# Kernel tuning notes

Measured on AMD Instinct MI355X. Metric: run time of the kernel, lower is better.

## Reference

```python
import jax, jax.numpy as jnp
import numpy as np

EPS = 1e-5

def _conv(x, w, b=None):
    # NCHW conv, stride 1, padding 1 (SAME for 3x3)
    y = jax.lax.conv_general_dilated(x, w, window_strides=(1, 1),
                                     padding=((1, 1), (1, 1)),
                                     dimension_numbers=('NCHW', 'OIHW', 'NCHW'))
    if b is not None:
        y = y + b[None, :, None, None]
    return y


def setup_inputs() -> dict:
    key = jax.random.key(0)
    ks = jax.random.split(key, 8)
    B, H, W = 4, 512, 640
    depth = jax.random.uniform(ks[0], (B, 1, H, W), dtype=jnp.float32) * 100.0
    img_feature = jax.random.normal(ks[1], (B, 16, H, W), dtype=jnp.float32)
    w1 = jax.random.normal(ks[2], (32, 16, 3, 3), dtype=jnp.float32) * 0.05
    b1 = jax.random.normal(ks[3], (32,), dtype=jnp.float32) * 0.05
    gamma = jnp.ones((32,), dtype=jnp.float32)
    beta = jnp.zeros((32,), dtype=jnp.float32)
    rmean = jax.random.normal(ks[4], (32,), dtype=jnp.float32) * 0.05
    rvar = jax.random.uniform(ks[5], (32,), dtype=jnp.float32) + 0.5
    w2 = jax.random.normal(ks[6], (9, 32, 3, 3), dtype=jnp.float32) * 0.05
    return {"depth": depth, "img_feature": img_feature, "w1": w1, "b1": b1,
            "gamma": gamma, "beta": beta, "rmean": rmean, "rvar": rvar, "w2": w2}


def reference(depth, img_feature, w1, b1, gamma, beta, rmean, rvar, w2):
    B, _, H, W = depth.shape
    # depth_propagation_layer: conv -> BN (eval, running stats) -> relu -> conv
    h1 = _conv(img_feature, w1, b1)
    h1 = (h1 - rmean[None, :, None, None]) * (gamma[None, :, None, None]
          * jax.lax.rsqrt(rvar + EPS)[None, :, None, None]) + beta[None, :, None, None]
    h1 = jax.nn.relu(h1)
    logits = _conv(h1, w2)                    # [B, 9, H, W]
    prob = jax.nn.softmax(logits, axis=1)     # per-pixel 3x3 filter weights
    dp = jnp.pad(depth, ((0, 0), (0, 0), (1, 1), (1, 1)), mode='edge')  # [B,1,H+2,W+2]
    patches = jnp.concatenate([dp[:, :, i:i + H, j:j + W]
                               for i in range(3) for j in range(3)], axis=1)  # [B,9,H,W]
    result_depth = jnp.sum(patches * prob, axis=1)  # [B, H, W]
    return result_depth
```

## Files before the change

kernel.cpp:

```cpp
#include <hip/hip_runtime.h>
#include <hip/hip_bf16.h>

#define HH 512
#define WW 640
#define HW (HH*WW)
#define NT 256
#define IMPLANEP (468*8 + 8)
#define H1PLANEP (360*8 + 8)

typedef short short8  __attribute__((ext_vector_type(8)));
typedef short short4v __attribute__((ext_vector_type(4)));
typedef float f32x16  __attribute__((ext_vector_type(16)));
typedef float f32x4   __attribute__((ext_vector_type(4)));

__device__ inline short f2bf(float f) {
    __hip_bfloat16 h = __float2bfloat16(f);
    short s; __builtin_memcpy(&s, &h, 2);
    return s;
}

__global__ void prep_weights(const float* __restrict__ w1, const float* __restrict__ b1,
                             const float* __restrict__ gamma, const float* __restrict__ beta,
                             const float* __restrict__ rmean, const float* __restrict__ rvar,
                             const float* __restrict__ w2,
                             short* __restrict__ ws_w1, short* __restrict__ ws_w2)
{
    int tid = blockIdx.x*blockDim.x + threadIdx.x;
    int stride = gridDim.x*blockDim.x;
    for (int i = tid; i < 4608; i += stride) {
        int oc = i / 144, rem = i - oc*144, c = rem / 9, t = rem - c*9;
        float a = gamma[oc] * rsqrtf(rvar[oc] + 1e-5f);
        ws_w1[t*512 + oc*16 + c] = f2bf(w1[i] * a);
    }
    for (int i = tid; i < 512; i += stride) {
        int oc = i >> 4, c = i & 15;
        float a = gamma[oc] * rsqrtf(rvar[oc] + 1e-5f);
        float bias = beta[oc] + (b1[oc] - rmean[oc]) * a;
        ws_w1[9*512 + i] = (c == 0) ? f2bf(bias) : (short)0;
    }
    for (int i = tid; i < 4608; i += stride) {
        int t = i >> 9, f = (i >> 5) & 15, c = i & 31;
        float val = (f < 9) ? w2[(f*32 + c)*9 + t] : 0.f;
        ws_w2[i] = f2bf(val);
    }
}

__launch_bounds__(NT, 4)
__global__ void fastprop_main(const float* __restrict__ depth,
                              const float* __restrict__ img,
                              const short* __restrict__ ws_w1,
                              const short* __restrict__ ws_w2,
                              float* __restrict__ out)
{
    __shared__ short s_img[2*IMPLANEP];
    __shared__ short s_h1 [4*H1PLANEP];
    __shared__ float s_depth[340];

    const int tid = threadIdx.x;

    int nid = blockIdx.x;
    int oid = (nid & 7)*640 + (nid >> 3);
    int bz = oid / 1280; int rem = oid - bz*1280;
    int by = rem / 20;   int bx = rem - by*20;
    const int gy0 = by*8, gx0 = bx*32;

    const float* imgb = img   + (size_t)bz*16*HW;
    const float* dpb  = depth + (size_t)bz*HW;

    const int lane = tid & 63;
    const int wid  = tid >> 6;

    const int oc = lane & 31, cg = lane >> 5;
    short8 a1[10];
    #pragma unroll
    for (int t = 0; t < 10; ++t)
        a1[t] = *(const short8*)&ws_w1[t*512 + oc*16 + cg*8];
    short8 bb = (short8)0;
    bb[0] = (cg == 0) ? (short)0x3F80 : (short)0;

    for (int g = tid; g < 936; g += NT) {
        int pixel = g >> 1, half = g & 1;
        int iy = pixel / 36, ix = pixel - iy*36;
        int gy = gy0 + iy - 2, gx = gx0 + ix - 2;
        bool v = ((unsigned)gy < HH) && ((unsigned)gx < WW);
        int cy = min(max(gy, 0), HH-1), cx = min(max(gx, 0), WW-1);
        const float* p = imgb + (size_t)(half*8)*HW + cy*WW + cx;
        float m = v ? 1.f : 0.f;
        short8 vv;
        #pragma unroll
        for (int c = 0; c < 8; ++c) vv[c] = f2bf(m * p[c*HW]);
        *(short8*)&s_img[half*IMPLANEP + pixel*8] = vv;
    }
    #pragma unroll
    for (int it = 0; it < 2; ++it) {
        int idx = tid + it*NT;
        if (idx < 340) {
            int ty = idx / 34, tx = idx - ty*34;
            int gy = min(max(gy0 + ty - 1, 0), HH-1);
            int gx = min(max(gx0 + tx - 1, 0), WW-1);
            s_depth[idx] = dpb[gy*WW + gx];
        }
    }
    __syncthreads();

    {
        const int OFS1[9] = {0, 8, 16, 288, 296, 304, 576, 584, 592};
        const int px = lane & 31;

        #pragma unroll
        for (int gi = 0; gi < 3; ++gi) {
            int g    = wid + gi*4;
            int hp   = g*32 + px;
            int base = cg*IMPLANEP + hp*8;
            f32x16 acc;
            #pragma unroll
            for (int i = 0; i < 16; ++i) acc[i] = 0.f;
            acc = __builtin_amdgcn_mfma_f32_32x32x16_bf16(a1[9], bb, acc, 0, 0, 0);
            #pragma unroll
            for (int t = 0; t < 9; ++t)
                acc = __builtin_amdgcn_mfma_f32_32x32x16_bf16(
                         a1[t], *(const short8*)&s_img[base + OFS1[t]], acc, 0, 0, 0);

            if (hp < 360) {
                unsigned hy = (unsigned)hp / 36u;
                int hx = hp - (int)hy*36;
                int gy = gy0 + (int)hy - 1, gx = gx0 + hx - 1;
                bool inb = ((unsigned)gy < HH) && ((unsigned)gx < WW);
                #pragma unroll
                for (int q = 0; q < 4; ++q) {
                    short4v h;
                    #pragma unroll
                    for (int j = 0; j < 4; ++j) {
                        float hv = fmaxf(acc[q*4 + j], 0.f);
                        h[j] = inb ? f2bf(hv) : (short)0;
                    }
                    *(short4v*)&s_h1[q*H1PLANEP + hp*8 + 4*cg] = h;
                }
            }
        }
    }
    __syncthreads();

    {
        const int fl = lane & 15, cg2 = lane >> 4;
        short8 a2[9];
        #pragma unroll
        for (int t = 0; t < 9; ++t)
            a2[t] = *(const short8*)&ws_w2[t*512 + fl*32 + cg2*8];

        const int r0 = 2*wid;

        #pragma unroll
        for (int chh = 0; chh < 2; ++chh) {
            const int ox0 = chh*16;
            const int colbase = cg2*H1PLANEP + (ox0 + fl)*8;

            short8 F[4][3];
            #pragma unroll
            for (int i = 0; i < 3; ++i)
                #pragma unroll
                for (int dx = 0; dx < 3; ++dx)
                    F[i][dx] = *(const short8*)&s_h1[colbase + ((r0 + i)*36 + dx)*8];
            #pragma unroll
            for (int dx = 0; dx < 3; ++dx)
                F[3][dx] = *(const short8*)&s_h1[colbase + ((r0 + 3)*36 + dx)*8];

            f32x4 acc0, acc1;
            #pragma unroll
            for (int i = 0; i < 4; ++i) { acc0[i] = 0.f; acc1[i] = 0.f; }
            #pragma unroll
            for (int ty = 0; ty < 3; ++ty)
                #pragma unroll
                for (int tx = 0; tx < 3; ++tx)
                    acc0 = __builtin_amdgcn_mfma_f32_16x16x32_bf16(
                             a2[ty*3 + tx], F[ty][tx], acc0, 0, 0, 0);
            #pragma unroll
            for (int ty = 0; ty < 3; ++ty)
                #pragma unroll
                for (int tx = 0; tx < 3; ++tx)
                    acc1 = __builtin_amdgcn_mfma_f32_16x16x32_bf16(
                             a2[ty*3 + tx], F[ty + 1][tx], acc1, 0, 0, 0);

            #pragma unroll
            for (int rr = 0; rr < 2; ++rr) {
                f32x4 lg = rr ? acc1 : acc0;
                int oy = r0 + rr, ox = ox0 + fl;
                float num = 0.f, den = 0.f;
                #pragma unroll
                for (int r = 0; r < 4; ++r) {
                    int f = cg2*4 + r;
                    if (f < 9) {
                        float e = __expf(lg[r]);
                        int fy = f/3, fx = f - fy*3;
                        float d = s_depth[(oy + fy)*34 + (ox + fx)];
                        den += e; num += e * d;
                    }
                }
                num += __shfl_xor(num, 16); den += __shfl_xor(den, 16);
                num += __shfl_xor(num, 32); den += __shfl_xor(den, 32);
                if (cg2 == 0)
                    out[(size_t)bz*HW + (size_t)(gy0 + oy)*WW + (gx0 + ox)] = num / den;
            }
        }
    }
}

extern "C" void kernel_launch(void* const* d_in, const int* in_sizes, int n_in,
                              void* d_out, int out_size, void* d_ws, size_t ws_size,
                              hipStream_t stream) {
    const float* depth = (const float*)d_in[0];
    const float* img   = (const float*)d_in[1];
    const float* w1    = (const float*)d_in[2];
    const float* b1    = (const float*)d_in[3];
    const float* gamma = (const float*)d_in[4];
    const float* beta  = (const float*)d_in[5];
    const float* rmean = (const float*)d_in[6];
    const float* rvar  = (const float*)d_in[7];
    const float* w2    = (const float*)d_in[8];
    float* out = (float*)d_out;

    short* ws_w1 = (short*)d_ws;
    short* ws_w2 = ws_w1 + 5120;

    prep_weights<<<16, NT, 0, stream>>>(w1, b1, gamma, beta, rmean, rvar, w2,
                                        ws_w1, ws_w2);
    fastprop_main<<<5120, NT, 0, stream>>>(depth, img, ws_w1, ws_w2, out);
}
```

Measured before the change: 63.41 us.

## Make blocks persistent over five tiles with register prefetch of next tile

The grid shrinks from 5120 to 1024 blocks, and each block loops over five consecutive tiles. While the current tile's MFMA convolutions and softmax run, the next tile's image and depth values are loaded from global memory into registers. The staged image halo drops from 13 rows to the 12 actually needed, which cuts global loads. This targets global-load latency exposed between the load and compute phases. The cost is many more live registers for the prefetch buffers, which may hurt occupancy, and the last MFMA group now reads stale shared memory past the image plane, which is only safe because those outputs are discarded.

```diff
diff --git a/kernel.cpp b/kernel.cpp
--- a/kernel.cpp
+++ b/kernel.cpp
@@ -5,7 +5,7 @@
 #define WW 640
 #define HW (HH*WW)
 #define NT 256
-#define IMPLANEP (468*8 + 8)
+#define IMPLANEP (432*8 + 8)
 #define H1PLANEP (360*8 + 8)
 
 typedef short short8  __attribute__((ext_vector_type(8)));
@@ -56,150 +56,187 @@
     __shared__ short s_h1 [4*H1PLANEP];
     __shared__ float s_depth[340];
 
-    const int tid = threadIdx.x;
-
-    int nid = blockIdx.x;
-    int oid = (nid & 7)*640 + (nid >> 3);
-    int bz = oid / 1280; int rem = oid - bz*1280;
-    int by = rem / 20;   int bx = rem - by*20;
-    const int gy0 = by*8, gx0 = bx*32;
-
-    const float* imgb = img   + (size_t)bz*16*HW;
-    const float* dpb  = depth + (size_t)bz*HW;
-
+    const int tid  = threadIdx.x;
     const int lane = tid & 63;
     const int wid  = tid >> 6;
 
-    const int oc = lane & 31, cg = lane >> 5;
-    short8 a1[10];
+    const int nid      = blockIdx.x;
+    const int base_oid = (nid & 7)*640 + (nid >> 3)*5;
+
+    int PIX[4], HALF[4], IY[4], IX[4]; bool ACT[4];
     #pragma unroll
-    for (int t = 0; t < 10; ++t)
-        a1[t] = *(const short8*)&ws_w1[t*512 + oc*16 + cg*8];
-    short8 bb = (short8)0;
-    bb[0] = (cg == 0) ? (short)0x3F80 : (short)0;
-
-    for (int g = tid; g < 936; g += NT) {
-        int pixel = g >> 1, half = g & 1;
-        int iy = pixel / 36, ix = pixel - iy*36;
-        int gy = gy0 + iy - 2, gx = gx0 + ix - 2;
-        bool v = ((unsigned)gy < HH) && ((unsigned)gx < WW);
-        int cy = min(max(gy, 0), HH-1), cx = min(max(gx, 0), WW-1);
-        const float* p = imgb + (size_t)(half*8)*HW + cy*WW + cx;
-        float m = v ? 1.f : 0.f;
-        short8 vv;
+    for (int j = 0; j < 4; ++j) {
+        int g = tid + j*NT;
+        ACT[j]  = (g < 864);
+        int pixel = g >> 1;
+        PIX[j]  = pixel; HALF[j] = g & 1;
+        IY[j]   = pixel / 36; IX[j] = pixel - 36*(pixel/36);
+    }
+
+    float r[4][8]; float msk[4]; float d0 = 0.f, d1 = 0.f;
+
+    auto load_tile = [&](int oid) {
+        int bz = oid / 1280; int rm = oid - bz*1280;
+        int by = rm / 20;    int bx = rm - by*20;
+        int gy0 = by*8, gx0 = bx*32;
+        const float* imgb = img   + (size_t)bz*16*HW;
+        const float* dpb  = depth + (size_t)bz*HW;
         #pragma unroll
-        for (int c = 0; c < 8; ++c) vv[c] = f2bf(m * p[c*HW]);
-        *(short8*)&s_img[half*IMPLANEP + pixel*8] = vv;
-    }
-    #pragma unroll
-    for (int it = 0; it < 2; ++it) {
-        int idx = tid + it*NT;
-        if (idx < 340) {
-            int ty = idx / 34, tx = idx - ty*34;
+        for (int j = 0; j < 4; ++j) {
+            if (ACT[j]) {
+                int gy = gy0 + IY[j] - 2, gx = gx0 + IX[j] - 2;
+                bool v = ((unsigned)gy < HH) && ((unsigned)gx < WW);
+                int cy = min(max(gy, 0), HH-1), cx = min(max(gx, 0), WW-1);
+                const float* p = imgb + (size_t)(HALF[j]*8)*HW + cy*WW + cx;
+                msk[j] = v ? 1.f : 0.f;
+                #pragma unroll
+                for (int c = 0; c < 8; ++c) r[j][c] = p[c*HW];
+            }
+        }
+        {
+            int ty = tid / 34, tx = tid - ty*34;
             int gy = min(max(gy0 + ty - 1, 0), HH-1);
             int gx = min(max(gx0 + tx - 1, 0), WW-1);
-            s_depth[idx] = dpb[gy*WW + gx];
-        }
-    }
-    __syncthreads();
-
-    {
-        const int OFS1[9] = {0, 8, 16, 288, 296, 304, 576, 584, 592};
-        const int px = lane & 31;
+            d0 = dpb[gy*WW + gx];
+        }
+        if (tid < 84) {
+            int i1 = tid + 256;
+            int ty = i1 / 34, tx = i1 - ty*34;
+            int gy = min(max(gy0 + ty - 1, 0), HH-1);
+            int gx = min(max(gx0 + tx - 1, 0), WW-1);
+            d1 = dpb[gy*WW + gx];
+        }
+    };
+
+    load_tile(base_oid);
+
+    for (int t = 0; t < 5; ++t) {
+        const int oid = base_oid + t;
+        int bz = oid / 1280; int rm = oid - bz*1280;
+        int by = rm / 20;    int bx = rm - by*20;
+        const int gy0 = by*8, gx0 = bx*32;
+
+        __syncthreads();
 
         #pragma unroll
-        for (int gi = 0; gi < 3; ++gi) {
-            int g    = wid + gi*4;
-            int hp   = g*32 + px;
-            int base = cg*IMPLANEP + hp*8;
-            f32x16 acc;
-            #pragma unroll
-            for (int i = 0; i < 16; ++i) acc[i] = 0.f;
-            acc = __builtin_amdgcn_mfma_f32_32x32x16_bf16(a1[9], bb, acc, 0, 0, 0);
-            #pragma unroll
-            for (int t = 0; t < 9; ++t)
-                acc = __builtin_amdgcn_mfma_f32_32x32x16_bf16(
-                         a1[t], *(const short8*)&s_img[base + OFS1[t]], acc, 0, 0, 0);
-
-            if (hp < 360) {
-                unsigned hy = (unsigned)hp / 36u;
-                int hx = hp - (int)hy*36;
-                int gy = gy0 + (int)hy - 1, gx = gx0 + hx - 1;
-                bool inb = ((unsigned)gy < HH) && ((unsigned)gx < WW);
-                #pragma unroll
-                for (int q = 0; q < 4; ++q) {
-                    short4v h;
-                    #pragma unroll
-                    for (int j = 0; j < 4; ++j) {
-                        float hv = fmaxf(acc[q*4 + j], 0.f);
-                        h[j] = inb ? f2bf(hv) : (short)0;
-                    }
-                    *(short4v*)&s_h1[q*H1PLANEP + hp*8 + 4*cg] = h;
-                }
-            }
-        }
-    }
-    __syncthreads();
-
-    {
-        const int fl = lane & 15, cg2 = lane >> 4;
-        short8 a2[9];
-        #pragma unroll
-        for (int t = 0; t < 9; ++t)
-            a2[t] = *(const short8*)&ws_w2[t*512 + fl*32 + cg2*8];
-
-        const int r0 = 2*wid;
-
-        #pragma unroll
-        for (int chh = 0; chh < 2; ++chh) {
-            const int ox0 = chh*16;
-            const int colbase = cg2*H1PLANEP + (ox0 + fl)*8;
-
-            short8 F[4][3];
-            #pragma unroll
-            for (int i = 0; i < 3; ++i)
-                #pragma unroll
-                for (int dx = 0; dx < 3; ++dx)
-                    F[i][dx] = *(const short8*)&s_h1[colbase + ((r0 + i)*36 + dx)*8];
-            #pragma unroll
-            for (int dx = 0; dx < 3; ++dx)
-                F[3][dx] = *(const short8*)&s_h1[colbase + ((r0 + 3)*36 + dx)*8];
-
-            f32x4 acc0, acc1;
-            #pragma unroll
-            for (int i = 0; i < 4; ++i) { acc0[i] = 0.f; acc1[i] = 0.f; }
-            #pragma unroll
-            for (int ty = 0; ty < 3; ++ty)
-                #pragma unroll
-                for (int tx = 0; tx < 3; ++tx)
-                    acc0 = __builtin_amdgcn_mfma_f32_16x16x32_bf16(
-                             a2[ty*3 + tx], F[ty][tx], acc0, 0, 0, 0);
-            #pragma unroll
-            for (int ty = 0; ty < 3; ++ty)
-                #pragma unroll
-                for (int tx = 0; tx < 3; ++tx)
-                    acc1 = __builtin_amdgcn_mfma_f32_16x16x32_bf16(
-                             a2[ty*3 + tx], F[ty + 1][tx], acc1, 0, 0, 0);
-
-            #pragma unroll
-            for (int rr = 0; rr < 2; ++rr) {
-                f32x4 lg = rr ? acc1 : acc0;
-                int oy = r0 + rr, ox = ox0 + fl;
-                float num = 0.f, den = 0.f;
-                #pragma unroll
-                for (int r = 0; r < 4; ++r) {
-                    int f = cg2*4 + r;
-                    if (f < 9) {
-                        float e = __expf(lg[r]);
-                        int fy = f/3, fx = f - fy*3;
-                        float d = s_depth[(oy + fy)*34 + (ox + fx)];
-                        den += e; num += e * d;
+        for (int j = 0; j < 4; ++j) {
+            if (ACT[j]) {
+                short8 vv;
+                #pragma unroll
+                for (int c = 0; c < 8; ++c) vv[c] = f2bf(msk[j] * r[j][c]);
+                *(short8*)&s_img[HALF[j]*IMPLANEP + PIX[j]*8] = vv;
+            }
+        }
+        s_depth[tid] = d0;
+        if (tid < 84) s_depth[tid + 256] = d1;
+
+        if (t < 4) load_tile(oid + 1);
+
+        __syncthreads();
+
+        {
+            const int oc = lane & 31, cg = lane >> 5;
+            short8 a1[10];
+            #pragma unroll
+            for (int tt = 0; tt < 10; ++tt)
+                a1[tt] = *(const short8*)&ws_w1[tt*512 + oc*16 + cg*8];
+            short8 bb = (short8)0;
+            bb[0] = (cg == 0) ? (short)0x3F80 : (short)0;
+
+            const int OFS1[9] = {0, 8, 16, 288, 296, 304, 576, 584, 592};
+            const int px = lane & 31;
+
+            #pragma unroll
+            for (int gi = 0; gi < 3; ++gi) {
+                int g    = wid + gi*4;
+                int hp   = g*32 + px;
+                int base = cg*IMPLANEP + hp*8;
+                f32x16 acc;
+                #pragma unroll
+                for (int i = 0; i < 16; ++i) acc[i] = 0.f;
+                acc = __builtin_amdgcn_mfma_f32_32x32x16_bf16(a1[9], bb, acc, 0, 0, 0);
+                #pragma unroll
+                for (int tt = 0; tt < 9; ++tt)
+                    acc = __builtin_amdgcn_mfma_f32_32x32x16_bf16(
+                             a1[tt], *(const short8*)&s_img[base + OFS1[tt]], acc, 0, 0, 0);
+
+                if (hp < 360) {
+                    unsigned hy = (unsigned)hp / 36u;
+                    int hx = hp - (int)hy*36;
+                    int gy = gy0 + (int)hy - 1, gx = gx0 + hx - 1;
+                    bool inb = ((unsigned)gy < HH) && ((unsigned)gx < WW);
+                    #pragma unroll
+                    for (int q = 0; q < 4; ++q) {
+                        short4v h;
+                        #pragma unroll
+                        for (int j = 0; j < 4; ++j) {
+                            float hv = fmaxf(acc[q*4 + j], 0.f);
+                            h[j] = inb ? f2bf(hv) : (short)0;
+                        }
+                        *(short4v*)&s_h1[q*H1PLANEP + hp*8 + 4*cg] = h;
                     }
                 }
-                num += __shfl_xor(num, 16); den += __shfl_xor(den, 16);
-                num += __shfl_xor(num, 32); den += __shfl_xor(den, 32);
-                if (cg2 == 0)
-                    out[(size_t)bz*HW + (size_t)(gy0 + oy)*WW + (gx0 + ox)] = num / den;
+            }
+        }
+        __syncthreads();
+
+        {
+            const int fl = lane & 15, cg2 = lane >> 4;
+            short8 a2[9];
+            #pragma unroll
+            for (int tt = 0; tt < 9; ++tt)
+                a2[tt] = *(const short8*)&ws_w2[tt*512 + fl*32 + cg2*8];
+
+            const int r0 = 2*wid;
+
+            #pragma unroll
+            for (int chh = 0; chh < 2; ++chh) {
+                const int ox0 = chh*16;
+                const int colbase = cg2*H1PLANEP + (ox0 + fl)*8;
+
+                short8 F[4][3];
+                #pragma unroll
+                for (int i = 0; i < 4; ++i)
+                    #pragma unroll
+                    for (int dx = 0; dx < 3; ++dx)
+                        F[i][dx] = *(const short8*)&s_h1[colbase + ((r0 + i)*36 + dx)*8];
+
+                f32x4 acc0, acc1;
+                #pragma unroll
+                for (int i = 0; i < 4; ++i) { acc0[i] = 0.f; acc1[i] = 0.f; }
+                #pragma unroll
+                for (int i = 0; i < 3; ++i)
+                    #pragma unroll
+                    for (int dx = 0; dx < 3; ++dx)
+                        acc0 = __builtin_amdgcn_mfma_f32_16x16x32_bf16(
+                                 a2[i*3 + dx], F[i][dx], acc0, 0, 0, 0);
+                #pragma unroll
+                for (int i = 0; i < 3; ++i)
+                    #pragma unroll
+                    for (int dx = 0; dx < 3; ++dx)
+                        acc1 = __builtin_amdgcn_mfma_f32_16x16x32_bf16(
+                                 a2[i*3 + dx], F[i + 1][dx], acc1, 0, 0, 0);
+
+                #pragma unroll
+                for (int rr = 0; rr < 2; ++rr) {
+                    f32x4 lg = rr ? acc1 : acc0;
+                    int oy = r0 + rr, ox = ox0 + fl;
+                    float num = 0.f, den = 0.f;
+                    #pragma unroll
+                    for (int q = 0; q < 4; ++q) {
+                        int f = cg2*4 + q;
+                        if (f < 9) {
+                            float e = __expf(lg[q]);
+                            int fy = f/3, fx = f - fy*3;
+                            float d = s_depth[(oy + fy)*34 + (ox + fx)];
+                            den += e; num += e * d;
+                        }
+                    }
+                    num += __shfl_xor(num, 16); den += __shfl_xor(den, 16);
+                    num += __shfl_xor(num, 32); den += __shfl_xor(den, 32);
+                    if (cg2 == 0)
+                        out[(size_t)bz*HW + (size_t)(gy0 + oy)*WW + (gx0 + ox)] = num / den;
+                }
             }
         }
     }
@@ -222,7 +259,7 @@
     short* ws_w1 = (short*)d_ws;
     short* ws_w2 = ws_w1 + 5120;
 
-    prep_weights<<<16, NT, 0, stream>>>(w1, b1, gamma, beta, rmean, rvar, w2,
-                                        ws_w1, ws_w2);
-    fastprop_main<<<5120, NT, 0, stream>>>(depth, img, ws_w1, ws_w2, out);
-}
+    prep_weights<<<16, 256, 0, stream>>>(w1, b1, gamma, beta, rmean, rvar, w2,
+                                         ws_w1, ws_w2);
+    fastprop_main<<<1024, NT, 0, stream>>>(depth, img, ws_w1, ws_w2, out);
+}
```

New measurement: 175.3 us. 176% more time.
